# Performance work log

Hardware: AMD Instinct MI355X
Metric: run time of the kernel (lower is better)

Reference implementation:

```python
import jax, jax.numpy as jnp
import numpy as np

N = 50000
E = 600000
IN_C = 128
OUT_C = 128
HEADS = 8
HEAD_C = OUT_C // HEADS  # 16


def setup_inputs() -> dict:
    key = jax.random.key(0)
    k1, k2, k3, k4, k5 = jax.random.split(key, 5)
    node_features = jax.random.normal(k1, (N, IN_C), dtype=jnp.float32)
    edge_index = jax.random.randint(k2, (2, E), 0, N, dtype=jnp.int64)
    # Xavier-ish scaled params
    W = jax.random.normal(k3, (OUT_C, IN_C), dtype=jnp.float32) * (1.0 / np.sqrt(IN_C))
    a_left = jax.random.normal(k4, (HEAD_C, HEADS, 1), dtype=jnp.float32) * (1.0 / np.sqrt(HEAD_C))
    a_right = jax.random.normal(k5, (HEAD_C, HEADS, 1), dtype=jnp.float32) * (1.0 / np.sqrt(HEAD_C))
    bias = jnp.zeros((OUT_C,), dtype=jnp.float32)
    return {"node_features": node_features, "edge_index": edge_index,
            "W": W, "a_left": a_left, "a_right": a_right, "bias": bias}


def reference(node_features, edge_index, W, a_left, a_right, bias):
    # Linear embedding (no bias), reshape to heads: n (h c) -> n h c
    emb = (node_features @ W.T).reshape(N, HEADS, HEAD_C)
    # Per-node attention scores
    src_scores = jnp.einsum('nhc,chi->nh', emb, a_left)
    tgt_scores = jnp.einsum('nhc,chi->nh', emb, a_right)
    src, trg = edge_index[0], edge_index[1]
    # Lift to edges, LeakyReLU(0.2)
    edge_scores = jax.nn.leaky_relu(src_scores[src] + tgt_scores[trg], negative_slope=0.2)  # [E, H]
    # Neighbourhood softmax via scatter-add over target nodes (matches exp/sum form)
    exp_scores = jnp.exp(edge_scores)
    denom = jax.ops.segment_sum(exp_scores, trg, num_segments=N)  # [N, H]
    attn = exp_scores / (denom[trg] + 1e-16)  # [E, H]
    # Weighted aggregation of lifted source embeddings
    weighted = emb[src] * attn[..., None]  # [E, H, C]
    out = jax.ops.segment_sum(weighted, trg, num_segments=N)  # [N, H, C]
    # concat heads + bias
    return out.reshape(N, HEADS * HEAD_C) + bias
```

## Files before the change

kernel.cpp:

```cpp
#include <hip/hip_runtime.h>

#define NN 50000
#define EE 600000
#define CC 128
#define HH 8
#define ESTRIDE 150000
#define GB 782
#define HB 586
#define NBI (2 * HB)
#define NBN 196
#define MAXDEG 64
#define LOG2E 1.4426950408889634f

typedef unsigned int u32;
typedef unsigned short u16;
typedef __attribute__((ext_vector_type(8))) short short8;
typedef __attribute__((ext_vector_type(4))) float f32x4;

__device__ __forceinline__ float b2f(u32 u) { return __uint_as_float(u << 16); }
__device__ __forceinline__ u16 f2b(float f) {
  u32 x = __float_as_uint(f);
  return (u16)((x + 0x7fffu + ((x >> 16) & 1u)) >> 16);
}
__device__ __forceinline__ u32 cvtpk(float lo, float hi) {
  u32 r;
  asm volatile("v_cvt_pk_bf16_f32 %0, %1, %2" : "=v"(r) : "v"(lo), "v"(hi));
  return r;
}

enum : int {
  OFF_FLAG = 0,
  OFF_CNT  = 64,
  OFF_WB   = OFF_CNT + NN + 64,
  OFF_SL   = OFF_WB + 8192,
  OFF_SR   = OFF_SL + NN * HH,
  OFF_SSRC = OFF_SR + NN * HH,
  OFF_EMB  = OFF_SSRC + NN * MAXDEG / 2 + 64,
  WS_WORDS = OFF_EMB + NN * 64
};

__global__ __launch_bounds__(256) void k_prep(const int* __restrict__ ei, const float* __restrict__ W,
                                              int* __restrict__ flag, int* __restrict__ cnt,
                                              u32* __restrict__ Wb) {
  int i = blockIdx.x * 256 + threadIdx.x;
  if (i < NN) cnt[i] = 0;
  if (i < CC * CC / 2) {
    float2 v = ((const float2*)W)[i];
    Wb[i] = (u32)f2b(v.x) | ((u32)f2b(v.y) << 16);
  }
  if (blockIdx.x == 0) {
    __shared__ int any;
    if (threadIdx.x == 0) any = 0;
    __syncthreads();
    int nz = 0;
    for (int k = threadIdx.x; k < 1024; k += 256) nz |= (ei[2 * k + 1] != 0) ? 1 : 0;
    if (nz) any = 1;
    __syncthreads();
    if (threadIdx.x == 0) flag[0] = any;
  }
}

__device__ __forceinline__ int swz(int row, int byte_in_row) {
  return ((row * 256 + byte_in_row) ^ ((row & 7) << 4));
}

__global__ __launch_bounds__(256) void k_gemm_hist(const float* __restrict__ X,
                                                   const u32* __restrict__ Wb,
                                                   const float* __restrict__ al,
                                                   const float* __restrict__ ar,
                                                   const int* __restrict__ ei,
                                                   const int* __restrict__ flag,
                                                   int* __restrict__ cnt,
                                                   u16* __restrict__ ssrc,
                                                   u32* __restrict__ emb,
                                                   float* __restrict__ sl, float* __restrict__ sr) {
  __shared__ unsigned char lds[32768];
  const int tid = threadIdx.x;
  const int b = blockIdx.x;

  if (b < NBI && (b & 1)) {
    const int et = (b >> 1) * 256 + tid;
    if (et < ESTRIDE) {
      const int f = flag[0];
      int s[4], t[4];
      if (f) {
#pragma unroll
        for (int k = 0; k < 4; ++k) {
          s[k] = ei[et + k * ESTRIDE];
          t[k] = ei[EE + et + k * ESTRIDE];
        }
      } else {
#pragma unroll
        for (int k = 0; k < 4; ++k) {
          s[k] = ((const int2*)ei)[et + k * ESTRIDE].x;
          t[k] = ((const int2*)ei)[EE + et + k * ESTRIDE].x;
        }
      }
#pragma unroll
      for (int k = 0; k < 4; ++k) {
        int r = atomicAdd(&cnt[t[k]], 1);
        if (r < MAXDEG) ssrc[(t[k] << 6) + r] = (u16)s[k];
      }
    }
    return;
  }

  const int tile = (b < NBI) ? (b >> 1) : (HB + (b - NBI));
  const int n0 = tile * 64;
  const int lane = tid & 63;
  const int w = tid >> 6;
  const int cwh16 = lane & 15, kg = lane >> 4;

  const int myrow = n0 + w * 16 + cwh16;
  float4 xa[8];
  {
    const float4* X4 = (const float4*)X;
    const bool ok = myrow < NN;
    const int base = myrow * 32 + kg * 2;
#pragma unroll
    for (int kk = 0; kk < 4; ++kk) {
      xa[2 * kk]     = ok ? X4[base + kk * 8]     : make_float4(0.f, 0.f, 0.f, 0.f);
      xa[2 * kk + 1] = ok ? X4[base + kk * 8 + 1] : make_float4(0.f, 0.f, 0.f, 0.f);
    }
  }

#pragma unroll
  for (int i = 0; i < 8; ++i) {
    int idx = tid + i * 256;
    int r = idx >> 4, c16 = idx & 15;
    uint4 v = ((const uint4*)Wb)[idx];
    *(uint4*)&lds[swz(r, c16 * 16)] = v;
  }
  __syncthreads();

  f32x4 acc[8];
#pragma unroll
  for (int nt = 0; nt < 8; ++nt) acc[nt] = (f32x4){0.f, 0.f, 0.f, 0.f};

  union { u32 u[4]; short8 s8; } pa;
#pragma unroll
  for (int kk = 0; kk < 4; ++kk) {
    pa.u[0] = cvtpk(xa[2 * kk].x, xa[2 * kk].y);
    pa.u[1] = cvtpk(xa[2 * kk].z, xa[2 * kk].w);
    pa.u[2] = cvtpk(xa[2 * kk + 1].x, xa[2 * kk + 1].y);
    pa.u[3] = cvtpk(xa[2 * kk + 1].z, xa[2 * kk + 1].w);
    const short8 a = pa.s8;
    const int kb = kk * 64 + kg * 16;
#pragma unroll
    for (int nt = 0; nt < 8; ++nt) {
      short8 bfr = *(const short8*)&lds[swz(nt * 16 + cwh16, kb)];
      acc[nt] = __builtin_amdgcn_mfma_f32_16x16x32_bf16(a, bfr, acc[nt], 0, 0, 0);
    }
  }

  __syncthreads();
#pragma unroll
  for (int nt = 0; nt < 8; ++nt) {
    const int col = nt * 16 + cwh16;
#pragma unroll
    for (int reg = 0; reg < 4; ++reg) {
      const int r = w * 16 + kg * 4 + reg;
      *(u16*)&lds[swz(r, col * 2)] = f2b(acc[nt][reg]);
    }
  }
  __syncthreads();

  {
    const int r = tid >> 2, hp = tid & 3;
    const int n = n0 + r;
    if (n < NN) {
      float sAl = 0.f, sAr = 0.f, sBl = 0.f, sBr = 0.f;
#pragma unroll
      for (int j = 0; j < 2; ++j) {
        uint4 q = *(const uint4*)&lds[swz(r, hp * 64 + j * 16)];
        u32 qq[4] = {q.x, q.y, q.z, q.w};
        const int h = 2 * hp;
#pragma unroll
        for (int u = 0; u < 4; ++u) {
          int cwh = j * 8 + 2 * u;
          float lo = b2f(qq[u] & 0xffffu), hi = b2f(qq[u] >> 16);
          sAl = fmaf(lo, al[cwh * 8 + h], sAl);       sAr = fmaf(lo, ar[cwh * 8 + h], sAr);
          sAl = fmaf(hi, al[(cwh + 1) * 8 + h], sAl); sAr = fmaf(hi, ar[(cwh + 1) * 8 + h], sAr);
        }
      }
#pragma unroll
      for (int j = 0; j < 2; ++j) {
        uint4 q = *(const uint4*)&lds[swz(r, hp * 64 + 32 + j * 16)];
        u32 qq[4] = {q.x, q.y, q.z, q.w};
        const int h = 2 * hp + 1;
#pragma unroll
        for (int u = 0; u < 4; ++u) {
          int cwh = j * 8 + 2 * u;
          float lo = b2f(qq[u] & 0xffffu), hi = b2f(qq[u] >> 16);
          sBl = fmaf(lo, al[cwh * 8 + h], sBl);       sBr = fmaf(lo, ar[cwh * 8 + h], sBr);
          sBl = fmaf(hi, al[(cwh + 1) * 8 + h], sBl); sBr = fmaf(hi, ar[(cwh + 1) * 8 + h], sBr);
        }
      }
      ((float2*)&sl[n * HH])[hp] = make_float2(sAl * LOG2E, sBl * LOG2E);
      ((float2*)&sr[n * HH])[hp] = make_float2(sAr * LOG2E, sBr * LOG2E);
    }
  }

#pragma unroll
  for (int i = 0; i < 4; ++i) {
    int idx = tid + i * 256;
    int r = idx >> 4, c16 = idx & 15;
    int n = n0 + r;
    if (n < NN) {
      uint4 v = *(const uint4*)&lds[swz(r, c16 * 16)];
      *((uint4*)(emb + n * 64 + c16 * 4)) = v;
    }
  }
}

__global__ __launch_bounds__(256) void k_agg(const u32* __restrict__ emb,
                                             const float* __restrict__ sl, const float* __restrict__ sr,
                                             const int* __restrict__ cnt, const u16* __restrict__ ssrc,
                                             const float* __restrict__ bias, float* __restrict__ out) {
  const int t = (blockIdx.x * 256 + threadIdx.x) >> 6;
  const int lane = threadIdx.x & 63;
  if (t >= NN) return;
  const int deg = cnt[t];
  const int base = t << 6;
  const int half = lane >> 5;
  const int l5 = lane & 31;
  const int h2 = l5 >> 2;
  const float sr2 = sr[t * HH + h2];
  const uint2* emb2 = (const uint2*)emb;
  float a0 = 0.f, a1 = 0.f, a2 = 0.f, a3 = 0.f, den = 0.f;
  for (int e = 0; e < deg; e += 16) {
    const int j0 = e + half * 8;
    uint4 raw = *(const uint4*)&ssrc[base + j0];
    u32 rw[4] = {raw.x, raw.y, raw.z, raw.w};
    int s[8];
    bool val[8];
#pragma unroll
    for (int k = 0; k < 8; ++k) {
      val[k] = (j0 + k) < deg;
      int sv = (int)((rw[k >> 1] >> ((k & 1) * 16)) & 0xffffu);
      s[k] = val[k] ? sv : 0;
    }
    float v[8];
#pragma unroll
    for (int k = 0; k < 8; ++k) v[k] = sl[s[k] * HH + h2];
    uint2 p[8];
#pragma unroll
    for (int k = 0; k < 8; ++k) p[k] = emb2[s[k] * 32 + l5];
#pragma unroll
    for (int k = 0; k < 8; ++k) {
      float vv = v[k] + sr2;
      vv = fmaxf(vv, 0.2f * vv);
      float w = exp2f(vv);
      w = val[k] ? w : 0.f;
      den += w;
      a0 = fmaf(w, b2f(p[k].x & 0xffffu), a0);
      a1 = fmaf(w, b2f(p[k].x >> 16), a1);
      a2 = fmaf(w, b2f(p[k].y & 0xffffu), a2);
      a3 = fmaf(w, b2f(p[k].y >> 16), a3);
    }
  }
  a0 += __shfl_xor(a0, 32);
  a1 += __shfl_xor(a1, 32);
  a2 += __shfl_xor(a2, 32);
  a3 += __shfl_xor(a3, 32);
  den += __shfl_xor(den, 32);
  if (half == 0) {
    const float inv = 1.f / (den + 1e-16f);
    float4 bv = ((const float4*)bias)[l5];
    ((float4*)out)[t * 32 + l5] =
        make_float4(fmaf(a0, inv, bv.x), fmaf(a1, inv, bv.y),
                    fmaf(a2, inv, bv.z), fmaf(a3, inv, bv.w));
  }
}

extern "C" void kernel_launch(void* const* d_in, const int* in_sizes, int n_in,
                              void* d_out, int out_size, void* d_ws, size_t ws_size,
                              hipStream_t stream) {
  const float* X  = (const float*)d_in[0];
  const int*   EI = (const int*)d_in[1];
  const float* W  = (const float*)d_in[2];
  const float* AL = (const float*)d_in[3];
  const float* AR = (const float*)d_in[4];
  const float* B  = (const float*)d_in[5];
  float* out = (float*)d_out;
  u32* ws = (u32*)d_ws;

  int*   flag = (int*)(ws + OFF_FLAG);
  int*   cnt  = (int*)(ws + OFF_CNT);
  u32*   Wb   = (u32*)(ws + OFF_WB);
  float* sl   = (float*)(ws + OFF_SL);
  float* sr   = (float*)(ws + OFF_SR);
  u16*   ssrc = (u16*)(ws + OFF_SSRC);
  u32*   emb  = (u32*)(ws + OFF_EMB);

  k_prep<<<NBN, 256, 0, stream>>>(EI, W, flag, cnt, Wb);
  k_gemm_hist<<<GB + HB, 256, 0, stream>>>(X, Wb, AL, AR, EI, flag, cnt, ssrc, emb, sl, sr);
  k_agg<<<(NN * 64 + 255) / 256, 256, 0, stream>>>(emb, sl, sr, cnt, ssrc, B, out);
}
```

Baseline: 79.85 us.

## Process two 64-row tiles per GEMM block to amortize W staging

Each GEMM block now computes 128 node rows (two 64-row sub-tiles) instead of 64, so the bf16 W matrix is loaded into LDS half as often and the total GEMM block count is halved. The interleaving of GEMM and histogram blocks is remapped so that even blocks below the boundary do GEMM and all remaining blocks do histogram. A launch_bounds minimum-occupancy hint of 4 is added. The cost is doubled accumulator registers per thread and fewer GEMM blocks to spread across CUs.

```diff
diff --git a/kernel.cpp b/kernel.cpp
--- a/kernel.cpp
+++ b/kernel.cpp
@@ -5,9 +5,9 @@
 #define CC 128
 #define HH 8
 #define ESTRIDE 150000
-#define GB 782
+#define GB2 391
 #define HB 586
-#define NBI (2 * HB)
+#define NBI2 (2 * GB2)
 #define NBN 196
 #define MAXDEG 64
 #define LOG2E 1.4426950408889634f
@@ -64,22 +64,24 @@
   return ((row * 256 + byte_in_row) ^ ((row & 7) << 4));
 }
 
-__global__ __launch_bounds__(256) void k_gemm_hist(const float* __restrict__ X,
-                                                   const u32* __restrict__ Wb,
-                                                   const float* __restrict__ al,
-                                                   const float* __restrict__ ar,
-                                                   const int* __restrict__ ei,
-                                                   const int* __restrict__ flag,
-                                                   int* __restrict__ cnt,
-                                                   u16* __restrict__ ssrc,
-                                                   u32* __restrict__ emb,
-                                                   float* __restrict__ sl, float* __restrict__ sr) {
+__global__ __launch_bounds__(256, 4) void k_gemm_hist(const float* __restrict__ X,
+                                                      const u32* __restrict__ Wb,
+                                                      const float* __restrict__ al,
+                                                      const float* __restrict__ ar,
+                                                      const int* __restrict__ ei,
+                                                      const int* __restrict__ flag,
+                                                      int* __restrict__ cnt,
+                                                      u16* __restrict__ ssrc,
+                                                      u32* __restrict__ emb,
+                                                      float* __restrict__ sl, float* __restrict__ sr) {
   __shared__ unsigned char lds[32768];
   const int tid = threadIdx.x;
   const int b = blockIdx.x;
 
-  if (b < NBI && (b & 1)) {
-    const int et = (b >> 1) * 256 + tid;
+  const bool isHist = (b < NBI2) ? (b & 1) : true;
+  if (isHist) {
+    const int hchunk = (b < NBI2) ? (b >> 1) : (b - NBI2 + GB2);
+    const int et = hchunk * 256 + tid;
     if (et < ESTRIDE) {
       const int f = flag[0];
       int s[4], t[4];
@@ -105,18 +107,17 @@
     return;
   }
 
-  const int tile = (b < NBI) ? (b >> 1) : (HB + (b - NBI));
-  const int n0 = tile * 64;
+  const int n0 = (b >> 1) * 128;
   const int lane = tid & 63;
   const int w = tid >> 6;
   const int cwh16 = lane & 15, kg = lane >> 4;
-
-  const int myrow = n0 + w * 16 + cwh16;
+  const float4* X4 = (const float4*)X;
+
+  const int row0 = n0 + w * 16 + cwh16;
   float4 xa[8];
   {
-    const float4* X4 = (const float4*)X;
-    const bool ok = myrow < NN;
-    const int base = myrow * 32 + kg * 2;
+    const bool ok = row0 < NN;
+    const int base = row0 * 32 + kg * 2;
 #pragma unroll
     for (int kk = 0; kk < 4; ++kk) {
       xa[2 * kk]     = ok ? X4[base + kk * 8]     : make_float4(0.f, 0.f, 0.f, 0.f);
@@ -133,9 +134,12 @@
   }
   __syncthreads();
 
-  f32x4 acc[8];
-#pragma unroll
-  for (int nt = 0; nt < 8; ++nt) acc[nt] = (f32x4){0.f, 0.f, 0.f, 0.f};
+  f32x4 acc0[8], acc1[8];
+#pragma unroll
+  for (int nt = 0; nt < 8; ++nt) {
+    acc0[nt] = (f32x4){0.f, 0.f, 0.f, 0.f};
+    acc1[nt] = (f32x4){0.f, 0.f, 0.f, 0.f};
+  }
 
   union { u32 u[4]; short8 s8; } pa;
 #pragma unroll
@@ -149,7 +153,32 @@
 #pragma unroll
     for (int nt = 0; nt < 8; ++nt) {
       short8 bfr = *(const short8*)&lds[swz(nt * 16 + cwh16, kb)];
-      acc[nt] = __builtin_amdgcn_mfma_f32_16x16x32_bf16(a, bfr, acc[nt], 0, 0, 0);
+      acc0[nt] = __builtin_amdgcn_mfma_f32_16x16x32_bf16(a, bfr, acc0[nt], 0, 0, 0);
+    }
+  }
+
+  const int row1 = n0 + 64 + w * 16 + cwh16;
+  {
+    const bool ok = row1 < NN;
+    const int base = row1 * 32 + kg * 2;
+#pragma unroll
+    for (int kk = 0; kk < 4; ++kk) {
+      xa[2 * kk]     = ok ? X4[base + kk * 8]     : make_float4(0.f, 0.f, 0.f, 0.f);
+      xa[2 * kk + 1] = ok ? X4[base + kk * 8 + 1] : make_float4(0.f, 0.f, 0.f, 0.f);
+    }
+  }
+#pragma unroll
+  for (int kk = 0; kk < 4; ++kk) {
+    pa.u[0] = cvtpk(xa[2 * kk].x, xa[2 * kk].y);
+    pa.u[1] = cvtpk(xa[2 * kk].z, xa[2 * kk].w);
+    pa.u[2] = cvtpk(xa[2 * kk + 1].x, xa[2 * kk + 1].y);
+    pa.u[3] = cvtpk(xa[2 * kk + 1].z, xa[2 * kk + 1].w);
+    const short8 a = pa.s8;
+    const int kb = kk * 64 + kg * 16;
+#pragma unroll
+    for (int nt = 0; nt < 8; ++nt) {
+      short8 bfr = *(const short8*)&lds[swz(nt * 16 + cwh16, kb)];
+      acc1[nt] = __builtin_amdgcn_mfma_f32_16x16x32_bf16(a, bfr, acc1[nt], 0, 0, 0);
     }
   }
 
@@ -160,19 +189,22 @@
 #pragma unroll
     for (int reg = 0; reg < 4; ++reg) {
       const int r = w * 16 + kg * 4 + reg;
-      *(u16*)&lds[swz(r, col * 2)] = f2b(acc[nt][reg]);
+      *(u16*)&lds[swz(r, col * 2)] = f2b(acc0[nt][reg]);
+      *(u16*)&lds[16384 + swz(r, col * 2)] = f2b(acc1[nt][reg]);
     }
   }
   __syncthreads();
 
-  {
+#pragma unroll
+  for (int sc = 0; sc < 2; ++sc) {
     const int r = tid >> 2, hp = tid & 3;
-    const int n = n0 + r;
+    const int n = n0 + sc * 64 + r;
+    const int rb = sc * 16384;
     if (n < NN) {
       float sAl = 0.f, sAr = 0.f, sBl = 0.f, sBr = 0.f;
 #pragma unroll
       for (int j = 0; j < 2; ++j) {
-        uint4 q = *(const uint4*)&lds[swz(r, hp * 64 + j * 16)];
+        uint4 q = *(const uint4*)&lds[rb + swz(r, hp * 64 + j * 16)];
         u32 qq[4] = {q.x, q.y, q.z, q.w};
         const int h = 2 * hp;
 #pragma unroll
@@ -185,7 +217,7 @@
       }
 #pragma unroll
       for (int j = 0; j < 2; ++j) {
-        uint4 q = *(const uint4*)&lds[swz(r, hp * 64 + 32 + j * 16)];
+        uint4 q = *(const uint4*)&lds[rb + swz(r, hp * 64 + 32 + j * 16)];
         u32 qq[4] = {q.x, q.y, q.z, q.w};
         const int h = 2 * hp + 1;
 #pragma unroll
@@ -202,12 +234,12 @@
   }
 
 #pragma unroll
-  for (int i = 0; i < 4; ++i) {
+  for (int i = 0; i < 8; ++i) {
     int idx = tid + i * 256;
     int r = idx >> 4, c16 = idx & 15;
     int n = n0 + r;
     if (n < NN) {
-      uint4 v = *(const uint4*)&lds[swz(r, c16 * 16)];
+      uint4 v = *(const uint4*)&lds[(r >> 6) * 16384 + swz(r & 63, c16 * 16)];
       *((uint4*)(emb + n * 64 + c16 * 4)) = v;
     }
   }
@@ -294,6 +326,6 @@
   u32*   emb  = (u32*)(ws + OFF_EMB);
 
   k_prep<<<NBN, 256, 0, stream>>>(EI, W, flag, cnt, Wb);
-  k_gemm_hist<<<GB + HB, 256, 0, stream>>>(X, Wb, AL, AR, EI, flag, cnt, ssrc, emb, sl, sr);
+  k_gemm_hist<<<GB2 + HB, 256, 0, stream>>>(X, Wb, AL, AR, EI, flag, cnt, ssrc, emb, sl, sr);
   k_agg<<<(NN * 64 + 255) / 256, 256, 0, stream>>>(emb, sl, sr, cnt, ssrc, B, out);
 }
```

After: 82.60 us. 3.4% more time.
